# Performance work log

Measured on AMD Instinct MI355X. Metric: run time of the kernel, lower is better.

Reference implementation:

```python
import jax, jax.numpy as jnp
import numpy as np

NUM_HEADS = 8
NEG_LARGE = -1e9  # stands in for -inf under the causal mask; masked entries get exactly 0 entmax weight


def _entmax15(z):
    """Exact 1.5-entmax along the last axis (Peters & Martins 2019 sort-based algorithm)."""
    z = z * 0.5
    zs = -jnp.sort(-z, axis=-1)                      # descending sort
    T = z.shape[-1]
    k = jnp.arange(1, T + 1, dtype=z.dtype)
    mean = jnp.cumsum(zs, axis=-1) / k
    mean_sq = jnp.cumsum(zs * zs, axis=-1) / k
    ss = k * (mean_sq - mean * mean)
    delta = (1.0 - ss) / k
    tau = mean - jnp.sqrt(jnp.maximum(delta, 0.0))
    support = jnp.sum(tau <= zs, axis=-1, keepdims=True)      # support size >= 1
    tau_star = jnp.take_along_axis(tau, support - 1, axis=-1)
    return jnp.square(jnp.maximum(z - tau_star, 0.0))


def setup_inputs() -> dict:
    key = jax.random.key(0)
    ks = jax.random.split(key, 9)
    B, T, D, H = 2, 2048, 512, NUM_HEADS
    dk = D // H
    s = 1.0 / np.sqrt(D)
    so = 1.0 / np.sqrt(dk)
    x = jax.random.normal(ks[0], (B, T, D), jnp.float32)
    Wq = jax.random.uniform(ks[1], (D, D), jnp.float32, -s, s)
    bq = jax.random.uniform(ks[2], (D,), jnp.float32, -s, s)
    Wk = jax.random.uniform(ks[3], (D, D), jnp.float32, -s, s)
    bk = jax.random.uniform(ks[4], (D,), jnp.float32, -s, s)
    Wv = jax.random.uniform(ks[5], (D, D), jnp.float32, -s, s)
    bv = jax.random.uniform(ks[6], (D,), jnp.float32, -s, s)
    Wo = jax.random.uniform(ks[7], (dk, D), jnp.float32, -so, so)
    bo = jax.random.uniform(ks[8], (D,), jnp.float32, -so, so)
    return {"x": x, "Wq": Wq, "bq": bq, "Wk": Wk, "bk": bk, "Wv": Wv, "bv": bv, "Wo": Wo, "bo": bo}


def reference(x, Wq, bq, Wk, bk, Wv, bv, Wo, bo):
    B, T, D = x.shape
    H = NUM_HEADS
    dk = D // H
    Q = (x @ Wq + bq).reshape(B, T, H, dk).transpose(0, 2, 1, 3)   # [B,H,T,dk]
    K = (x @ Wk + bk).reshape(B, T, H, dk).transpose(0, 2, 1, 3)
    V = (x @ Wv + bv).reshape(B, T, H, dk).transpose(0, 2, 1, 3)
    scores = jnp.einsum('bhtd,bhsd->bhts', Q, K) / np.float32(np.sqrt(dk))
    causal = jnp.triu(jnp.ones((T, T), bool), k=1)                 # True above diagonal
    scores = jnp.where(causal[None, None, :, :], jnp.float32(NEG_LARGE), scores)
    weights = _entmax15(scores)                                    # [B,H,T,T]
    weights_avg = weights.mean(axis=1)                             # [B,T,T]
    V_combined = V.mean(axis=1)                                    # [B,T,dk]
    out = jnp.einsum('bts,bsd->btd', weights_avg, V_combined)      # [B,T,dk]
    return out @ Wo + bo, weights_avg
```

## Files before the change

kernel.cpp:

```cpp
#include <hip/hip_runtime.h>
#include <hip/hip_bf16.h>
#include <cstdint>

#define B_ 2
#define T_ 2048
#define D_ 512
#define H_ 8
#define DK_ 64
#define TQ_ 8
#define NTL_ (T_ / TQ_)
#define M_ (B_ * T_)

__global__ __launch_bounds__(256) void gemm_bias_kernel(
    const float* __restrict__ A, const float* __restrict__ W,
    const float* __restrict__ bias, float* __restrict__ C,
    int M, int N, int K)
{
  __shared__ float As[32][68];
  __shared__ float Bs[32][68];
  const int bm = blockIdx.y * 64;
  const int bn = blockIdx.x * 64;
  const int tid = threadIdx.x;
  const int tx = tid & 15, ty = tid >> 4;
  float acc[4][4] = {};
  for (int k0 = 0; k0 < K; k0 += 32) {
    {
      const int r = tid >> 2;
      const int c = (tid & 3) << 2;
      const float4 a0 = *reinterpret_cast<const float4*>(&A[(size_t)(bm + r) * K + k0 + c]);
      const float4 a1 = *reinterpret_cast<const float4*>(&A[(size_t)(bm + r) * K + k0 + 16 + c]);
      As[c + 0][r] = a0.x;  As[c + 1][r] = a0.y;  As[c + 2][r] = a0.z;  As[c + 3][r] = a0.w;
      As[c + 16][r] = a1.x; As[c + 17][r] = a1.y; As[c + 18][r] = a1.z; As[c + 19][r] = a1.w;
    }
    {
      const int r = tid >> 4;
      const int c = (tid & 15) << 2;
      *reinterpret_cast<float4*>(&Bs[r][c]) =
          *reinterpret_cast<const float4*>(&W[(size_t)(k0 + r) * N + bn + c]);
      *reinterpret_cast<float4*>(&Bs[r + 16][c]) =
          *reinterpret_cast<const float4*>(&W[(size_t)(k0 + 16 + r) * N + bn + c]);
    }
    __syncthreads();
#pragma unroll
    for (int kk = 0; kk < 32; ++kk) {
      const float4 av = *reinterpret_cast<const float4*>(&As[kk][ty * 4]);
      const float4 bv = *reinterpret_cast<const float4*>(&Bs[kk][tx * 4]);
      acc[0][0] = fmaf(av.x, bv.x, acc[0][0]); acc[0][1] = fmaf(av.x, bv.y, acc[0][1]);
      acc[0][2] = fmaf(av.x, bv.z, acc[0][2]); acc[0][3] = fmaf(av.x, bv.w, acc[0][3]);
      acc[1][0] = fmaf(av.y, bv.x, acc[1][0]); acc[1][1] = fmaf(av.y, bv.y, acc[1][1]);
      acc[1][2] = fmaf(av.y, bv.z, acc[1][2]); acc[1][3] = fmaf(av.y, bv.w, acc[1][3]);
      acc[2][0] = fmaf(av.z, bv.x, acc[2][0]); acc[2][1] = fmaf(av.z, bv.y, acc[2][1]);
      acc[2][2] = fmaf(av.z, bv.z, acc[2][2]); acc[2][3] = fmaf(av.z, bv.w, acc[2][3]);
      acc[3][0] = fmaf(av.w, bv.x, acc[3][0]); acc[3][1] = fmaf(av.w, bv.y, acc[3][1]);
      acc[3][2] = fmaf(av.w, bv.z, acc[3][2]); acc[3][3] = fmaf(av.w, bv.w, acc[3][3]);
    }
    __syncthreads();
  }
#pragma unroll
  for (int i = 0; i < 4; ++i) {
    const int row = bm + ty * 4 + i;
#pragma unroll
    for (int j = 0; j < 4; ++j) {
      const int col = bn + tx * 4 + j;
      C[(size_t)row * N + col] = acc[i][j] + bias[col];
    }
  }
}

__global__ __launch_bounds__(256) void gemm_bias_kernelT(
    const float* __restrict__ A, const float* __restrict__ W,
    const float* __restrict__ bias, float* __restrict__ Ct,
    int M, int N, int K)
{
  __shared__ float As[32][68];
  __shared__ float Bs[32][68];
  const int bm = blockIdx.y * 64;
  const int bn = blockIdx.x * 64;
  const int tid = threadIdx.x;
  const int tx = tid & 15, ty = tid >> 4;
  float acc[4][4] = {};
  for (int k0 = 0; k0 < K; k0 += 32) {
    {
      const int r = tid >> 2;
      const int c = (tid & 3) << 2;
      const float4 a0 = *reinterpret_cast<const float4*>(&A[(size_t)(bm + r) * K + k0 + c]);
      const float4 a1 = *reinterpret_cast<const float4*>(&A[(size_t)(bm + r) * K + k0 + 16 + c]);
      As[c + 0][r] = a0.x;  As[c + 1][r] = a0.y;  As[c + 2][r] = a0.z;  As[c + 3][r] = a0.w;
      As[c + 16][r] = a1.x; As[c + 17][r] = a1.y; As[c + 18][r] = a1.z; As[c + 19][r] = a1.w;
    }
    {
      const int r = tid >> 4;
      const int c = (tid & 15) << 2;
      *reinterpret_cast<float4*>(&Bs[r][c]) =
          *reinterpret_cast<const float4*>(&W[(size_t)(k0 + r) * N + bn + c]);
      *reinterpret_cast<float4*>(&Bs[r + 16][c]) =
          *reinterpret_cast<const float4*>(&W[(size_t)(k0 + 16 + r) * N + bn + c]);
    }
    __syncthreads();
#pragma unroll
    for (int kk = 0; kk < 32; ++kk) {
      const float4 av = *reinterpret_cast<const float4*>(&As[kk][ty * 4]);
      const float4 bv = *reinterpret_cast<const float4*>(&Bs[kk][tx * 4]);
      acc[0][0] = fmaf(av.x, bv.x, acc[0][0]); acc[0][1] = fmaf(av.x, bv.y, acc[0][1]);
      acc[0][2] = fmaf(av.x, bv.z, acc[0][2]); acc[0][3] = fmaf(av.x, bv.w, acc[0][3]);
      acc[1][0] = fmaf(av.y, bv.x, acc[1][0]); acc[1][1] = fmaf(av.y, bv.y, acc[1][1]);
      acc[1][2] = fmaf(av.y, bv.z, acc[1][2]); acc[1][3] = fmaf(av.y, bv.w, acc[1][3]);
      acc[2][0] = fmaf(av.z, bv.x, acc[2][0]); acc[2][1] = fmaf(av.z, bv.y, acc[2][1]);
      acc[2][2] = fmaf(av.z, bv.z, acc[2][2]); acc[2][3] = fmaf(av.z, bv.w, acc[2][3]);
      acc[3][0] = fmaf(av.w, bv.x, acc[3][0]); acc[3][1] = fmaf(av.w, bv.y, acc[3][1]);
      acc[3][2] = fmaf(av.w, bv.z, acc[3][2]); acc[3][3] = fmaf(av.w, bv.w, acc[3][3]);
    }
    __syncthreads();
  }
#pragma unroll
  for (int j = 0; j < 4; ++j) {
    const int col = bn + tx * 4 + j;
    const float bb = bias[col];
    const float4 v = make_float4(acc[0][j] + bb, acc[1][j] + bb, acc[2][j] + bb, acc[3][j] + bb);
    *reinterpret_cast<float4*>(&Ct[(size_t)col * M + bm + ty * 4]) = v;
  }
}

__global__ __launch_bounds__(256) void vcombine_kernel(const float* __restrict__ V,
                                                       float* __restrict__ Vc)
{
  const int idx = blockIdx.x * 256 + threadIdx.x;
  if (idx >= M_ * DK_) return;
  const int row = idx >> 6, d = idx & 63;
  float s = 0.f;
#pragma unroll
  for (int h = 0; h < H_; ++h) s += V[(size_t)row * D_ + h * DK_ + d];
  Vc[idx] = s * 0.125f;
}

__global__ __launch_bounds__(512, 4)
void attn_kernel(
    const float* __restrict__ Qg, const float* __restrict__ Kt,
    const float* __restrict__ Vc, float* __restrict__ wavg,
    float* __restrict__ attn_out)
{
  __shared__ float sc[TQ_][T_];
  __shared__ float part[4][TQ_][DK_];

  const int tid = threadIdx.x;
  const int b = blockIdx.x & 1;
  const int tile = (NTL_ - 1) - (blockIdx.x >> 1);
  const int t0 = tile * TQ_;
  const int nS = t0 + TQ_;
  const int wave = __builtin_amdgcn_readfirstlane(tid >> 6);
  const int lane = tid & 63;
  const int n = t0 + wave + 1;
  float* const scw = &sc[wave][0];

  float wacc[32];
#pragma unroll
  for (int j = 0; j < 32; ++j) wacc[j] = 0.f;

  for (int h = 0; h < H_; ++h) {
    if (wave * 256 < nS) {
      const int s0 = min(tid * 4, nS - 4);
      const float* Ktp = &Kt[(size_t)(h * DK_) * M_ + b * T_ + s0];
      const float* Qp  = &Qg[(size_t)(b * T_ + t0) * D_ + h * DK_];
      float4 a[TQ_];
#pragma unroll
      for (int r = 0; r < TQ_; ++r) a[r] = make_float4(0.f, 0.f, 0.f, 0.f);
#pragma unroll 2
      for (int d4 = 0; d4 < 16; ++d4) {
        const float4 k0 = *reinterpret_cast<const float4*>(Ktp + (size_t)(d4 * 4 + 0) * M_);
        const float4 k1 = *reinterpret_cast<const float4*>(Ktp + (size_t)(d4 * 4 + 1) * M_);
        const float4 k2 = *reinterpret_cast<const float4*>(Ktp + (size_t)(d4 * 4 + 2) * M_);
        const float4 k3 = *reinterpret_cast<const float4*>(Ktp + (size_t)(d4 * 4 + 3) * M_);
#pragma unroll
        for (int r = 0; r < TQ_; ++r) {
          const float q0 = Qp[r * D_ + d4 * 4 + 0];
          const float q1 = Qp[r * D_ + d4 * 4 + 1];
          const float q2 = Qp[r * D_ + d4 * 4 + 2];
          const float q3 = Qp[r * D_ + d4 * 4 + 3];
          a[r].x = fmaf(q0, k0.x, a[r].x); a[r].y = fmaf(q0, k0.y, a[r].y);
          a[r].z = fmaf(q0, k0.z, a[r].z); a[r].w = fmaf(q0, k0.w, a[r].w);
          a[r].x = fmaf(q1, k1.x, a[r].x); a[r].y = fmaf(q1, k1.y, a[r].y);
          a[r].z = fmaf(q1, k1.z, a[r].z); a[r].w = fmaf(q1, k1.w, a[r].w);
          a[r].x = fmaf(q2, k2.x, a[r].x); a[r].y = fmaf(q2, k2.y, a[r].y);
          a[r].z = fmaf(q2, k2.z, a[r].z); a[r].w = fmaf(q2, k2.w, a[r].w);
          a[r].x = fmaf(q3, k3.x, a[r].x); a[r].y = fmaf(q3, k3.y, a[r].y);
          a[r].z = fmaf(q3, k3.z, a[r].z); a[r].w = fmaf(q3, k3.w, a[r].w);
        }
      }
#pragma unroll
      for (int r = 0; r < TQ_; ++r) {
        a[r].x *= 0.0625f; a[r].y *= 0.0625f; a[r].z *= 0.0625f; a[r].w *= 0.0625f;
        *reinterpret_cast<float4*>(&sc[r][s0]) = a[r];
      }
    }
    __syncthreads();

    float srow[32];
#pragma unroll
    for (int j = 0; j < 32; ++j) {
      if (j * 64 < n) {
        const int s = lane + j * 64;
        const float v = scw[s];
        srow[j] = (s < n) ? v : -1e30f;
      }
    }

    float mx = -1e30f;
#pragma unroll
    for (int j = 0; j < 32; ++j)
      if (j * 64 < n) mx = fmaxf(mx, srow[j]);
#pragma unroll
    for (int m = 32; m >= 1; m >>= 1) mx = fmaxf(mx, __shfl_xor(mx, m, 64));

    float tau = mx - 1.0f;
#pragma unroll 1
    for (int it = 0; it < 12; ++it) {
      float s1 = 0.f, s2 = 0.f, cn = 0.f;
#pragma unroll
      for (int j = 0; j < 32; ++j) {
        if (j * 64 < n) {
          const float u = fmaxf(srow[j] - tau, 0.f);
          s1 += u;
          s2 = fmaf(u, u, s2);
          cn += (u > 0.f) ? 1.f : 0.f;
        }
      }
#pragma unroll
      for (int m = 32; m >= 1; m >>= 1) {
        s1 += __shfl_xor(s1, m, 64);
        s2 += __shfl_xor(s2, m, 64);
      }
      if (fabsf(s2 - 1.0f) < 1e-5f) break;
      if (it < 3) {
#pragma unroll
        for (int m = 32; m >= 1; m >>= 1) cn += __shfl_xor(cn, m, 64);
        const float kf = fmaxf(cn, 1.f);
        const float mu = tau + s1 / kf;
        const float ss = s2 - s1 * s1 / kf;
        tau = mu - sqrtf(fmaxf((1.0f - ss) / kf, 0.f));
      } else {
        tau += (s2 - 1.0f) / fmaxf(2.f * s1, 1e-12f);
      }
    }
    tau = fminf(tau, mx - 1e-8f);

#pragma unroll
    for (int j = 0; j < 32; ++j) {
      if (j * 64 < n) {
        const float u = fmaxf(srow[j] - tau, 0.f);
        wacc[j] = fmaf(u, u, wacc[j]);
      }
    }
    __syncthreads();
  }

#pragma unroll
  for (int j = 0; j < 32; ++j) scw[lane + j * 64] = wacc[j];
  __syncthreads();

  for (int i4 = tid; i4 < TQ_ * T_ / 4; i4 += 512) {
    const int r = i4 >> 9;
    const int c4 = i4 & 511;
    float4 w = reinterpret_cast<const float4*>(&sc[r][0])[c4];
    w.x *= 0.125f; w.y *= 0.125f; w.z *= 0.125f; w.w *= 0.125f;
    reinterpret_cast<float4*>(&wavg[(size_t)(b * T_ + t0 + r) * T_])[c4] = w;
  }

  {
    const int sg = wave & 3;
    const int rb = (wave >> 2) * 4;
    float a0 = 0.f, a1 = 0.f, a2 = 0.f, a3 = 0.f;
    for (int s = sg; s < nS; s += 4) {
      const float v = Vc[(size_t)(b * T_ + s) * DK_ + lane];
      a0 += sc[rb + 0][s] * v;
      a1 += sc[rb + 1][s] * v;
      a2 += sc[rb + 2][s] * v;
      a3 += sc[rb + 3][s] * v;
    }
    part[sg][rb + 0][lane] = a0;
    part[sg][rb + 1][lane] = a1;
    part[sg][rb + 2][lane] = a2;
    part[sg][rb + 3][lane] = a3;
  }
  __syncthreads();
  {
    const int r = wave;
    const float o = (part[0][r][lane] + part[1][r][lane] +
                     part[2][r][lane] + part[3][r][lane]) * 0.125f;
    attn_out[(size_t)(b * T_ + t0 + r) * DK_ + lane] = o;
  }
}

extern "C" void kernel_launch(void* const* d_in, const int* in_sizes, int n_in,
                              void* d_out, int out_size, void* d_ws, size_t ws_size,
                              hipStream_t stream)
{
  const float* x  = (const float*)d_in[0];
  const float* Wq = (const float*)d_in[1];
  const float* bq = (const float*)d_in[2];
  const float* Wk = (const float*)d_in[3];
  const float* bk = (const float*)d_in[4];
  const float* Wv = (const float*)d_in[5];
  const float* bv = (const float*)d_in[6];
  const float* Wo = (const float*)d_in[7];
  const float* bo = (const float*)d_in[8];
  float* out = (float*)d_out;
  float* ws  = (float*)d_ws;

  float* Q  = ws;
  float* Kt = Q + (size_t)M_ * D_;
  float* V  = Kt + (size_t)D_ * M_;
  float* Vc = V + (size_t)M_ * D_;
  float* AO = Vc + (size_t)M_ * DK_;

  float* out1 = out;
  float* wavg = out + (size_t)M_ * D_;

  const dim3 gp(D_ / 64, M_ / 64);
  gemm_bias_kernel <<<gp, 256, 0, stream>>>(x, Wq, bq, Q,  M_, D_, D_);
  gemm_bias_kernelT<<<gp, 256, 0, stream>>>(x, Wk, bk, Kt, M_, D_, D_);
  gemm_bias_kernel <<<gp, 256, 0, stream>>>(x, Wv, bv, V,  M_, D_, D_);
  vcombine_kernel<<<(M_ * DK_ + 255) / 256, 256, 0, stream>>>(V, Vc);
  attn_kernel<<<B_ * NTL_, 512, 0, stream>>>(Q, Kt, Vc, wavg, AO);
  gemm_bias_kernel<<<gp, 256, 0, stream>>>(AO, Wo, bo, out1, M_, D_, DK_);
}
```

Before: 376.4 us.

## Warp-specialize attention: producer waves compute next head scores while consumers run entmax

Halves the query tile to four rows and double-buffers the score tile in shared memory. Waves 0-3 compute QK scores for head h+1 while waves 4-7 each run the entmax threshold iteration on one row for head h, so score computation overlaps with the serial entmax solve. This removes the phase where all waves sat idle waiting on either step. In exchange, twice as many blocks reload K per head with a smaller tile (less Q reuse), and half the waves idle in each role when the workloads are unbalanced.

```diff
diff --git a/kernel.cpp b/kernel.cpp
--- a/kernel.cpp
+++ b/kernel.cpp
@@ -7,7 +7,7 @@
 #define D_ 512
 #define H_ 8
 #define DK_ 64
-#define TQ_ 8
+#define TQ_ 4
 #define NTL_ (T_ / TQ_)
 #define M_ (B_ * T_)
 
@@ -139,7 +139,7 @@
     const float* __restrict__ Vc, float* __restrict__ wavg,
     float* __restrict__ attn_out)
 {
-  __shared__ float sc[TQ_][T_];
+  __shared__ float sc[2][TQ_][T_];
   __shared__ float part[4][TQ_][DK_];
 
   const int tid = threadIdx.x;
@@ -149,140 +149,153 @@
   const int nS = t0 + TQ_;
   const int wave = __builtin_amdgcn_readfirstlane(tid >> 6);
   const int lane = tid & 63;
-  const int n = t0 + wave + 1;
-  float* const scw = &sc[wave][0];
 
   float wacc[32];
 #pragma unroll
   for (int j = 0; j < 32; ++j) wacc[j] = 0.f;
 
+  auto score_head = [&](int h, int nb) {
+    const int stid = (wave << 6) | lane;
+    const float* Qp = &Qg[(size_t)(b * T_ + t0) * D_ + h * DK_];
+#pragma unroll 1
+    for (int c = 0; c < T_; c += 1024) {
+      if (c < nS) {
+        const int s0 = min(stid * 4 + c, nS - 4);
+        const float* Ktp = &Kt[(size_t)(h * DK_) * M_ + b * T_ + s0];
+        float4 a0 = {}, a1 = {}, a2 = {}, a3 = {};
+#pragma unroll 2
+        for (int d4 = 0; d4 < 16; ++d4) {
+          const float4 k0 = *reinterpret_cast<const float4*>(Ktp + (size_t)(d4 * 4 + 0) * M_);
+          const float4 k1 = *reinterpret_cast<const float4*>(Ktp + (size_t)(d4 * 4 + 1) * M_);
+          const float4 k2 = *reinterpret_cast<const float4*>(Ktp + (size_t)(d4 * 4 + 2) * M_);
+          const float4 k3 = *reinterpret_cast<const float4*>(Ktp + (size_t)(d4 * 4 + 3) * M_);
+#pragma unroll
+          for (int r = 0; r < TQ_; ++r) {
+            const float q0 = Qp[r * D_ + d4 * 4 + 0];
+            const float q1 = Qp[r * D_ + d4 * 4 + 1];
+            const float q2 = Qp[r * D_ + d4 * 4 + 2];
+            const float q3 = Qp[r * D_ + d4 * 4 + 3];
+            float4& a = (r == 0) ? a0 : (r == 1) ? a1 : (r == 2) ? a2 : a3;
+            a.x = fmaf(q0, k0.x, a.x); a.y = fmaf(q0, k0.y, a.y);
+            a.z = fmaf(q0, k0.z, a.z); a.w = fmaf(q0, k0.w, a.w);
+            a.x = fmaf(q1, k1.x, a.x); a.y = fmaf(q1, k1.y, a.y);
+            a.z = fmaf(q1, k1.z, a.z); a.w = fmaf(q1, k1.w, a.w);
+            a.x = fmaf(q2, k2.x, a.x); a.y = fmaf(q2, k2.y, a.y);
+            a.z = fmaf(q2, k2.z, a.z); a.w = fmaf(q2, k2.w, a.w);
+            a.x = fmaf(q3, k3.x, a.x); a.y = fmaf(q3, k3.y, a.y);
+            a.z = fmaf(q3, k3.z, a.z); a.w = fmaf(q3, k3.w, a.w);
+          }
+        }
+        a0.x *= 0.0625f; a0.y *= 0.0625f; a0.z *= 0.0625f; a0.w *= 0.0625f;
+        a1.x *= 0.0625f; a1.y *= 0.0625f; a1.z *= 0.0625f; a1.w *= 0.0625f;
+        a2.x *= 0.0625f; a2.y *= 0.0625f; a2.z *= 0.0625f; a2.w *= 0.0625f;
+        a3.x *= 0.0625f; a3.y *= 0.0625f; a3.z *= 0.0625f; a3.w *= 0.0625f;
+        *reinterpret_cast<float4*>(&sc[nb][0][s0]) = a0;
+        *reinterpret_cast<float4*>(&sc[nb][1][s0]) = a1;
+        *reinterpret_cast<float4*>(&sc[nb][2][s0]) = a2;
+        *reinterpret_cast<float4*>(&sc[nb][3][s0]) = a3;
+      }
+    }
+  };
+
+  if (wave < 4) score_head(0, 0);
+  __syncthreads();
+
+#pragma unroll 1
   for (int h = 0; h < H_; ++h) {
-    if (wave * 256 < nS) {
-      const int s0 = min(tid * 4, nS - 4);
-      const float* Ktp = &Kt[(size_t)(h * DK_) * M_ + b * T_ + s0];
-      const float* Qp  = &Qg[(size_t)(b * T_ + t0) * D_ + h * DK_];
-      float4 a[TQ_];
-#pragma unroll
-      for (int r = 0; r < TQ_; ++r) a[r] = make_float4(0.f, 0.f, 0.f, 0.f);
-#pragma unroll 2
-      for (int d4 = 0; d4 < 16; ++d4) {
-        const float4 k0 = *reinterpret_cast<const float4*>(Ktp + (size_t)(d4 * 4 + 0) * M_);
-        const float4 k1 = *reinterpret_cast<const float4*>(Ktp + (size_t)(d4 * 4 + 1) * M_);
-        const float4 k2 = *reinterpret_cast<const float4*>(Ktp + (size_t)(d4 * 4 + 2) * M_);
-        const float4 k3 = *reinterpret_cast<const float4*>(Ktp + (size_t)(d4 * 4 + 3) * M_);
-#pragma unroll
-        for (int r = 0; r < TQ_; ++r) {
-          const float q0 = Qp[r * D_ + d4 * 4 + 0];
-          const float q1 = Qp[r * D_ + d4 * 4 + 1];
-          const float q2 = Qp[r * D_ + d4 * 4 + 2];
-          const float q3 = Qp[r * D_ + d4 * 4 + 3];
-          a[r].x = fmaf(q0, k0.x, a[r].x); a[r].y = fmaf(q0, k0.y, a[r].y);
-          a[r].z = fmaf(q0, k0.z, a[r].z); a[r].w = fmaf(q0, k0.w, a[r].w);
-          a[r].x = fmaf(q1, k1.x, a[r].x); a[r].y = fmaf(q1, k1.y, a[r].y);
-          a[r].z = fmaf(q1, k1.z, a[r].z); a[r].w = fmaf(q1, k1.w, a[r].w);
-          a[r].x = fmaf(q2, k2.x, a[r].x); a[r].y = fmaf(q2, k2.y, a[r].y);
-          a[r].z = fmaf(q2, k2.z, a[r].z); a[r].w = fmaf(q2, k2.w, a[r].w);
-          a[r].x = fmaf(q3, k3.x, a[r].x); a[r].y = fmaf(q3, k3.y, a[r].y);
-          a[r].z = fmaf(q3, k3.z, a[r].z); a[r].w = fmaf(q3, k3.w, a[r].w);
+    if (wave < 4) {
+      if (h + 1 < H_) score_head(h + 1, (h + 1) & 1);
+    } else {
+      const int row = wave - 4;
+      const int n = t0 + row + 1;
+      const float* scw = &sc[h & 1][row][0];
+
+      float srow[32];
+      float mx = -1e30f;
+#pragma unroll
+      for (int j = 0; j < 32; ++j) {
+        if (j * 64 < n) {
+          const int s = lane + j * 64;
+          const float v = (s < n) ? scw[s] : -1e30f;
+          srow[j] = v;
+          mx = fmaxf(mx, v);
         }
       }
 #pragma unroll
-      for (int r = 0; r < TQ_; ++r) {
-        a[r].x *= 0.0625f; a[r].y *= 0.0625f; a[r].z *= 0.0625f; a[r].w *= 0.0625f;
-        *reinterpret_cast<float4*>(&sc[r][s0]) = a[r];
+      for (int m = 32; m >= 1; m >>= 1) mx = fmaxf(mx, __shfl_xor(mx, m, 64));
+
+      float tau = mx - 1.0f;
+#pragma unroll 1
+      for (int it = 0; it < 12; ++it) {
+        float s1 = 0.f, s2 = 0.f, cn = 0.f;
+#pragma unroll
+        for (int j = 0; j < 32; ++j) {
+          if (j * 64 < n) {
+            const float u = fmaxf(srow[j] - tau, 0.f);
+            s1 += u;
+            s2 = fmaf(u, u, s2);
+            cn += (u > 0.f) ? 1.f : 0.f;
+          }
+        }
+#pragma unroll
+        for (int m = 32; m >= 1; m >>= 1) {
+          s1 += __shfl_xor(s1, m, 64);
+          s2 += __shfl_xor(s2, m, 64);
+        }
+        if (fabsf(s2 - 1.0f) < 1e-5f) break;
+        if (it < 3) {
+#pragma unroll
+          for (int m = 32; m >= 1; m >>= 1) cn += __shfl_xor(cn, m, 64);
+          const float kf = fmaxf(cn, 1.f);
+          const float mu = tau + s1 / kf;
+          const float ss = s2 - s1 * s1 / kf;
+          tau = mu - sqrtf(fmaxf((1.0f - ss) / kf, 0.f));
+        } else {
+          tau += (s2 - 1.0f) / fmaxf(2.f * s1, 1e-12f);
+        }
       }
-    }
-    __syncthreads();
-
-    float srow[32];
-#pragma unroll
-    for (int j = 0; j < 32; ++j) {
-      if (j * 64 < n) {
-        const int s = lane + j * 64;
-        const float v = scw[s];
-        srow[j] = (s < n) ? v : -1e30f;
-      }
-    }
-
-    float mx = -1e30f;
-#pragma unroll
-    for (int j = 0; j < 32; ++j)
-      if (j * 64 < n) mx = fmaxf(mx, srow[j]);
-#pragma unroll
-    for (int m = 32; m >= 1; m >>= 1) mx = fmaxf(mx, __shfl_xor(mx, m, 64));
-
-    float tau = mx - 1.0f;
-#pragma unroll 1
-    for (int it = 0; it < 12; ++it) {
-      float s1 = 0.f, s2 = 0.f, cn = 0.f;
+      tau = fminf(tau, mx - 1e-8f);
+
 #pragma unroll
       for (int j = 0; j < 32; ++j) {
         if (j * 64 < n) {
           const float u = fmaxf(srow[j] - tau, 0.f);
-          s1 += u;
-          s2 = fmaf(u, u, s2);
-          cn += (u > 0.f) ? 1.f : 0.f;
+          wacc[j] = fmaf(u, u, wacc[j]);
         }
       }
-#pragma unroll
-      for (int m = 32; m >= 1; m >>= 1) {
-        s1 += __shfl_xor(s1, m, 64);
-        s2 += __shfl_xor(s2, m, 64);
-      }
-      if (fabsf(s2 - 1.0f) < 1e-5f) break;
-      if (it < 3) {
-#pragma unroll
-        for (int m = 32; m >= 1; m >>= 1) cn += __shfl_xor(cn, m, 64);
-        const float kf = fmaxf(cn, 1.f);
-        const float mu = tau + s1 / kf;
-        const float ss = s2 - s1 * s1 / kf;
-        tau = mu - sqrtf(fmaxf((1.0f - ss) / kf, 0.f));
-      } else {
-        tau += (s2 - 1.0f) / fmaxf(2.f * s1, 1e-12f);
-      }
-    }
-    tau = fminf(tau, mx - 1e-8f);
-
-#pragma unroll
-    for (int j = 0; j < 32; ++j) {
-      if (j * 64 < n) {
-        const float u = fmaxf(srow[j] - tau, 0.f);
-        wacc[j] = fmaf(u, u, wacc[j]);
-      }
-    }
-    __syncthreads();
-  }
-
-#pragma unroll
-  for (int j = 0; j < 32; ++j) scw[lane + j * 64] = wacc[j];
+    }
+    __syncthreads();
+  }
+
+  if (wave >= 4) {
+    const int row = wave - 4;
+#pragma unroll
+    for (int j = 0; j < 32; ++j) sc[0][row][lane + j * 64] = wacc[j];
+  }
   __syncthreads();
 
   for (int i4 = tid; i4 < TQ_ * T_ / 4; i4 += 512) {
     const int r = i4 >> 9;
     const int c4 = i4 & 511;
-    float4 w = reinterpret_cast<const float4*>(&sc[r][0])[c4];
+    float4 w = reinterpret_cast<const float4*>(&sc[0][r][0])[c4];
     w.x *= 0.125f; w.y *= 0.125f; w.z *= 0.125f; w.w *= 0.125f;
     reinterpret_cast<float4*>(&wavg[(size_t)(b * T_ + t0 + r) * T_])[c4] = w;
   }
 
   {
     const int sg = wave & 3;
-    const int rb = (wave >> 2) * 4;
-    float a0 = 0.f, a1 = 0.f, a2 = 0.f, a3 = 0.f;
+    const int rp = (wave >> 2) * 2;
+    float a0 = 0.f, a1 = 0.f;
     for (int s = sg; s < nS; s += 4) {
       const float v = Vc[(size_t)(b * T_ + s) * DK_ + lane];
-      a0 += sc[rb + 0][s] * v;
-      a1 += sc[rb + 1][s] * v;
-      a2 += sc[rb + 2][s] * v;
-      a3 += sc[rb + 3][s] * v;
-    }
-    part[sg][rb + 0][lane] = a0;
-    part[sg][rb + 1][lane] = a1;
-    part[sg][rb + 2][lane] = a2;
-    part[sg][rb + 3][lane] = a3;
+      a0 += sc[0][rp + 0][s] * v;
+      a1 += sc[0][rp + 1][s] * v;
+    }
+    part[sg][rp + 0][lane] = a0;
+    part[sg][rp + 1][lane] = a1;
   }
   __syncthreads();
-  {
+  if (wave < TQ_) {
     const int r = wave;
     const float o = (part[0][r][lane] + part[1][r][lane] +
                      part[2][r][lane] + part[3][r][lane]) * 0.125f;
```

Measured after the change: 533.9 us. 1.42x slower.

## Split attention per head with int16 scores, atomic weight accumulation, separate PV kernel

Applied to the files above, without the earlier changes.

The attention kernel is restructured so each block handles one head, one batch and a 4-row query tile. This multiplies the grid by the head count and shrinks shared memory by storing scores as quantized int16 in a scaled domain. Per-head entmax weights are accumulated into a pre-zeroed wavg buffer with sparse atomicAdds (only nonzero entries). The weights-times-V product moves to a new pv_kernel that reads wavg back from global memory. This adds a zeroing pass, atomic traffic and an extra global read of the 32MB weight matrix. The int16 quantization of scores (step 1/512) also risks accuracy loss.

```diff
diff --git a/kernel.cpp b/kernel.cpp
--- a/kernel.cpp
+++ b/kernel.cpp
@@ -7,9 +7,12 @@
 #define D_ 512
 #define H_ 8
 #define DK_ 64
-#define TQ_ 8
+#define TQ_ 4
 #define NTL_ (T_ / TQ_)
 #define M_ (B_ * T_)
+
+#define SSC_ 8192.0f
+#define S2_  (SSC_ * SSC_)
 
 __global__ __launch_bounds__(256) void gemm_bias_kernel(
     const float* __restrict__ A, const float* __restrict__ W,
@@ -133,160 +136,196 @@
   Vc[idx] = s * 0.125f;
 }
 
-__global__ __launch_bounds__(512, 4)
+__global__ __launch_bounds__(256) void zero_kernel(float4* __restrict__ p, int n4)
+{
+  const int stride = gridDim.x * 256;
+  const float4 z = make_float4(0.f, 0.f, 0.f, 0.f);
+  for (int i = blockIdx.x * 256 + threadIdx.x; i < n4; i += stride) p[i] = z;
+}
+
+__global__ __launch_bounds__(256, 6)
 void attn_kernel(
     const float* __restrict__ Qg, const float* __restrict__ Kt,
-    const float* __restrict__ Vc, float* __restrict__ wavg,
-    float* __restrict__ attn_out)
-{
-  __shared__ float sc[TQ_][T_];
-  __shared__ float part[4][TQ_][DK_];
+    float* __restrict__ wavg)
+{
+  __shared__ short ssc[TQ_][T_];
 
   const int tid = threadIdx.x;
-  const int b = blockIdx.x & 1;
-  const int tile = (NTL_ - 1) - (blockIdx.x >> 1);
+  const int bid = blockIdx.x;
+  const int h = bid >> 10;
+  const int b = (bid >> 9) & 1;
+  const int tile = (NTL_ - 1) - (bid & 511);
   const int t0 = tile * TQ_;
   const int nS = t0 + TQ_;
   const int wave = __builtin_amdgcn_readfirstlane(tid >> 6);
   const int lane = tid & 63;
-  const int n = t0 + wave + 1;
-  float* const scw = &sc[wave][0];
-
-  float wacc[32];
-#pragma unroll
-  for (int j = 0; j < 32; ++j) wacc[j] = 0.f;
-
-  for (int h = 0; h < H_; ++h) {
-    if (wave * 256 < nS) {
-      const int s0 = min(tid * 4, nS - 4);
-      const float* Ktp = &Kt[(size_t)(h * DK_) * M_ + b * T_ + s0];
-      const float* Qp  = &Qg[(size_t)(b * T_ + t0) * D_ + h * DK_];
-      float4 a[TQ_];
-#pragma unroll
-      for (int r = 0; r < TQ_; ++r) a[r] = make_float4(0.f, 0.f, 0.f, 0.f);
+
+  {
+    const float* Qp = &Qg[(size_t)(b * T_ + t0) * D_ + h * DK_];
+#pragma unroll 1
+    for (int c = 0; c < T_; c += 1024) {
+      if (c < nS) {
+        const int s0 = min(tid * 4 + c, nS - 4);
+        const float* Ktp = &Kt[(size_t)(h * DK_) * M_ + b * T_ + s0];
+        float4 a[TQ_];
+#pragma unroll
+        for (int r = 0; r < TQ_; ++r) a[r] = make_float4(0.f, 0.f, 0.f, 0.f);
 #pragma unroll 2
-      for (int d4 = 0; d4 < 16; ++d4) {
-        const float4 k0 = *reinterpret_cast<const float4*>(Ktp + (size_t)(d4 * 4 + 0) * M_);
-        const float4 k1 = *reinterpret_cast<const float4*>(Ktp + (size_t)(d4 * 4 + 1) * M_);
-        const float4 k2 = *reinterpret_cast<const float4*>(Ktp + (size_t)(d4 * 4 + 2) * M_);
-        const float4 k3 = *reinterpret_cast<const float4*>(Ktp + (size_t)(d4 * 4 + 3) * M_);
+        for (int d4 = 0; d4 < 16; ++d4) {
+          const float4 k0 = *reinterpret_cast<const float4*>(Ktp + (size_t)(d4 * 4 + 0) * M_);
+          const float4 k1 = *reinterpret_cast<const float4*>(Ktp + (size_t)(d4 * 4 + 1) * M_);
+          const float4 k2 = *reinterpret_cast<const float4*>(Ktp + (size_t)(d4 * 4 + 2) * M_);
+          const float4 k3 = *reinterpret_cast<const float4*>(Ktp + (size_t)(d4 * 4 + 3) * M_);
+#pragma unroll
+          for (int r = 0; r < TQ_; ++r) {
+            const float q0 = Qp[r * D_ + d4 * 4 + 0];
+            const float q1 = Qp[r * D_ + d4 * 4 + 1];
+            const float q2 = Qp[r * D_ + d4 * 4 + 2];
+            const float q3 = Qp[r * D_ + d4 * 4 + 3];
+            a[r].x = fmaf(q0, k0.x, a[r].x); a[r].y = fmaf(q0, k0.y, a[r].y);
+            a[r].z = fmaf(q0, k0.z, a[r].z); a[r].w = fmaf(q0, k0.w, a[r].w);
+            a[r].x = fmaf(q1, k1.x, a[r].x); a[r].y = fmaf(q1, k1.y, a[r].y);
+            a[r].z = fmaf(q1, k1.z, a[r].z); a[r].w = fmaf(q1, k1.w, a[r].w);
+            a[r].x = fmaf(q2, k2.x, a[r].x); a[r].y = fmaf(q2, k2.y, a[r].y);
+            a[r].z = fmaf(q2, k2.z, a[r].z); a[r].w = fmaf(q2, k2.w, a[r].w);
+            a[r].x = fmaf(q3, k3.x, a[r].x); a[r].y = fmaf(q3, k3.y, a[r].y);
+            a[r].z = fmaf(q3, k3.z, a[r].z); a[r].w = fmaf(q3, k3.w, a[r].w);
+          }
+        }
 #pragma unroll
         for (int r = 0; r < TQ_; ++r) {
-          const float q0 = Qp[r * D_ + d4 * 4 + 0];
-          const float q1 = Qp[r * D_ + d4 * 4 + 1];
-          const float q2 = Qp[r * D_ + d4 * 4 + 2];
-          const float q3 = Qp[r * D_ + d4 * 4 + 3];
-          a[r].x = fmaf(q0, k0.x, a[r].x); a[r].y = fmaf(q0, k0.y, a[r].y);
-          a[r].z = fmaf(q0, k0.z, a[r].z); a[r].w = fmaf(q0, k0.w, a[r].w);
-          a[r].x = fmaf(q1, k1.x, a[r].x); a[r].y = fmaf(q1, k1.y, a[r].y);
-          a[r].z = fmaf(q1, k1.z, a[r].z); a[r].w = fmaf(q1, k1.w, a[r].w);
-          a[r].x = fmaf(q2, k2.x, a[r].x); a[r].y = fmaf(q2, k2.y, a[r].y);
-          a[r].z = fmaf(q2, k2.z, a[r].z); a[r].w = fmaf(q2, k2.w, a[r].w);
-          a[r].x = fmaf(q3, k3.x, a[r].x); a[r].y = fmaf(q3, k3.y, a[r].y);
-          a[r].z = fmaf(q3, k3.z, a[r].z); a[r].w = fmaf(q3, k3.w, a[r].w);
+          const int i0 = __float2int_rn(fminf(fmaxf(a[r].x * 512.f, -32000.f), 32000.f));
+          const int i1 = __float2int_rn(fminf(fmaxf(a[r].y * 512.f, -32000.f), 32000.f));
+          const int i2 = __float2int_rn(fminf(fmaxf(a[r].z * 512.f, -32000.f), 32000.f));
+          const int i3 = __float2int_rn(fminf(fmaxf(a[r].w * 512.f, -32000.f), 32000.f));
+          short4 st; st.x = (short)i0; st.y = (short)i1; st.z = (short)i2; st.w = (short)i3;
+          *reinterpret_cast<short4*>(&ssc[r][s0]) = st;
         }
       }
-#pragma unroll
-      for (int r = 0; r < TQ_; ++r) {
-        a[r].x *= 0.0625f; a[r].y *= 0.0625f; a[r].z *= 0.0625f; a[r].w *= 0.0625f;
-        *reinterpret_cast<float4*>(&sc[r][s0]) = a[r];
+    }
+  }
+  __syncthreads();
+
+  const int t = t0 + wave;
+  const int n = t + 1;
+  float srow[32];
+
+#pragma unroll
+  for (int j = 0; j < 4; ++j) {
+    if (j * 512 < n) {
+      const uint4 pk = *reinterpret_cast<const uint4*>(&ssc[wave][j * 512 + lane * 8]);
+      const unsigned pw[4] = {pk.x, pk.y, pk.z, pk.w};
+#pragma unroll
+      for (int q = 0; q < 4; ++q) {
+        const int s_lo = j * 512 + lane * 8 + q * 2;
+        const float lo = (float)((int)(short)(pw[q] & 0xffffu));
+        const float hi = (float)((int)pw[q] >> 16);
+        srow[j * 8 + q * 2 + 0] = (s_lo + 0 < n) ? lo : -1e30f;
+        srow[j * 8 + q * 2 + 1] = (s_lo + 1 < n) ? hi : -1e30f;
       }
-    }
-    __syncthreads();
-
-    float srow[32];
-#pragma unroll
-    for (int j = 0; j < 32; ++j) {
-      if (j * 64 < n) {
-        const int s = lane + j * 64;
-        const float v = scw[s];
-        srow[j] = (s < n) ? v : -1e30f;
-      }
-    }
-
-    float mx = -1e30f;
-#pragma unroll
-    for (int j = 0; j < 32; ++j)
-      if (j * 64 < n) mx = fmaxf(mx, srow[j]);
-#pragma unroll
-    for (int m = 32; m >= 1; m >>= 1) mx = fmaxf(mx, __shfl_xor(mx, m, 64));
-
-    float tau = mx - 1.0f;
+    } else {
+#pragma unroll
+      for (int q = 0; q < 8; ++q) srow[j * 8 + q] = -1e30f;
+    }
+  }
+  asm volatile("" ::: "memory");
+
+  float mx = -1e30f;
+#pragma unroll
+  for (int i = 0; i < 32; ++i) mx = fmaxf(mx, srow[i]);
+#pragma unroll
+  for (int m = 32; m >= 1; m >>= 1) mx = fmaxf(mx, __shfl_xor(mx, m, 64));
+
+  float tau = mx - SSC_;
 #pragma unroll 1
-    for (int it = 0; it < 12; ++it) {
-      float s1 = 0.f, s2 = 0.f, cn = 0.f;
-#pragma unroll
-      for (int j = 0; j < 32; ++j) {
-        if (j * 64 < n) {
-          const float u = fmaxf(srow[j] - tau, 0.f);
+  for (int it = 0; it < 12; ++it) {
+    float s1 = 0.f, s2 = 0.f, cn = 0.f;
+#pragma unroll
+    for (int j = 0; j < 4; ++j) {
+      if (j * 512 < n) {
+#pragma unroll
+        for (int q = 0; q < 8; ++q) {
+          const float u = fmaxf(srow[j * 8 + q] - tau, 0.f);
           s1 += u;
           s2 = fmaf(u, u, s2);
           cn += (u > 0.f) ? 1.f : 0.f;
         }
       }
-#pragma unroll
-      for (int m = 32; m >= 1; m >>= 1) {
-        s1 += __shfl_xor(s1, m, 64);
-        s2 += __shfl_xor(s2, m, 64);
+    }
+#pragma unroll
+    for (int m = 32; m >= 1; m >>= 1) {
+      s1 += __shfl_xor(s1, m, 64);
+      s2 += __shfl_xor(s2, m, 64);
+    }
+    if (fabsf(s2 - S2_) < 672.f) break;
+    if (it < 3) {
+#pragma unroll
+      for (int m = 32; m >= 1; m >>= 1) cn += __shfl_xor(cn, m, 64);
+      const float kf = fmaxf(cn, 1.f);
+      const float mu = tau + s1 / kf;
+      const float ss = s2 - s1 * s1 / kf;
+      tau = mu - sqrtf(fmaxf((S2_ - ss) / kf, 0.f));
+    } else {
+      tau += (s2 - S2_) / fmaxf(2.f * s1, 1e-6f);
+    }
+  }
+  tau = fminf(tau, mx - 1.f);
+
+  const float wconv = 0.125f / (SSC_ * SSC_);
+  float* const wrow = &wavg[(size_t)(b * T_ + t) * T_];
+#pragma unroll
+  for (int j = 0; j < 4; ++j) {
+    if (j * 512 < n) {
+#pragma unroll
+      for (int q = 0; q < 8; ++q) {
+        const float u = fmaxf(srow[j * 8 + q] - tau, 0.f);
+        if (__any(u > 0.f)) {
+          if (u > 0.f) {
+            const int s = j * 512 + lane * 8 + q;
+            atomicAdd(&wrow[s], u * u * wconv);
+          }
+        }
       }
-      if (fabsf(s2 - 1.0f) < 1e-5f) break;
-      if (it < 3) {
-#pragma unroll
-        for (int m = 32; m >= 1; m >>= 1) cn += __shfl_xor(cn, m, 64);
-        const float kf = fmaxf(cn, 1.f);
-        const float mu = tau + s1 / kf;
-        const float ss = s2 - s1 * s1 / kf;
-        tau = mu - sqrtf(fmaxf((1.0f - ss) / kf, 0.f));
-      } else {
-        tau += (s2 - 1.0f) / fmaxf(2.f * s1, 1e-12f);
-      }
-    }
-    tau = fminf(tau, mx - 1e-8f);
-
-#pragma unroll
-    for (int j = 0; j < 32; ++j) {
-      if (j * 64 < n) {
-        const float u = fmaxf(srow[j] - tau, 0.f);
-        wacc[j] = fmaf(u, u, wacc[j]);
-      }
-    }
-    __syncthreads();
-  }
-
-#pragma unroll
-  for (int j = 0; j < 32; ++j) scw[lane + j * 64] = wacc[j];
-  __syncthreads();
-
-  for (int i4 = tid; i4 < TQ_ * T_ / 4; i4 += 512) {
-    const int r = i4 >> 9;
-    const int c4 = i4 & 511;
-    float4 w = reinterpret_cast<const float4*>(&sc[r][0])[c4];
-    w.x *= 0.125f; w.y *= 0.125f; w.z *= 0.125f; w.w *= 0.125f;
-    reinterpret_cast<float4*>(&wavg[(size_t)(b * T_ + t0 + r) * T_])[c4] = w;
-  }
-
-  {
-    const int sg = wave & 3;
-    const int rb = (wave >> 2) * 4;
-    float a0 = 0.f, a1 = 0.f, a2 = 0.f, a3 = 0.f;
-    for (int s = sg; s < nS; s += 4) {
-      const float v = Vc[(size_t)(b * T_ + s) * DK_ + lane];
-      a0 += sc[rb + 0][s] * v;
-      a1 += sc[rb + 1][s] * v;
-      a2 += sc[rb + 2][s] * v;
-      a3 += sc[rb + 3][s] * v;
-    }
-    part[sg][rb + 0][lane] = a0;
-    part[sg][rb + 1][lane] = a1;
-    part[sg][rb + 2][lane] = a2;
-    part[sg][rb + 3][lane] = a3;
-  }
+    }
+  }
+}
+
+__global__ __launch_bounds__(256) void pv_kernel(
+    const float* __restrict__ wavg, const float* __restrict__ Vc,
+    float* __restrict__ AO)
+{
+  __shared__ float part[4][TQ_][DK_];
+  const int tid = threadIdx.x;
+  const int m0 = blockIdx.x * TQ_;
+  const int b = m0 >> 11;
+  const int tl = m0 & (T_ - 1);
+  const int wave = __builtin_amdgcn_readfirstlane(tid >> 6);
+  const int lane = tid & 63;
+
+  const int smax = min((wave + 1) * 512, tl + TQ_);
+  float a0 = 0.f, a1 = 0.f, a2 = 0.f, a3 = 0.f;
+  const float* w0 = &wavg[(size_t)(m0 + 0) * T_];
+  const float* w1 = &wavg[(size_t)(m0 + 1) * T_];
+  const float* w2 = &wavg[(size_t)(m0 + 2) * T_];
+  const float* w3 = &wavg[(size_t)(m0 + 3) * T_];
+#pragma unroll 1
+  for (int s = wave * 512; s < smax; ++s) {
+    const float v = Vc[(size_t)(b * T_ + s) * DK_ + lane];
+    a0 = fmaf(w0[s], v, a0);
+    a1 = fmaf(w1[s], v, a1);
+    a2 = fmaf(w2[s], v, a2);
+    a3 = fmaf(w3[s], v, a3);
+  }
+  part[wave][0][lane] = a0;
+  part[wave][1][lane] = a1;
+  part[wave][2][lane] = a2;
+  part[wave][3][lane] = a3;
   __syncthreads();
   {
     const int r = wave;
-    const float o = (part[0][r][lane] + part[1][r][lane] +
-                     part[2][r][lane] + part[3][r][lane]) * 0.125f;
-    attn_out[(size_t)(b * T_ + t0 + r) * DK_ + lane] = o;
+    const float o = part[0][r][lane] + part[1][r][lane] +
+                    part[2][r][lane] + part[3][r][lane];
+    AO[(size_t)(m0 + r) * DK_ + lane] = o;
   }
 }
 
@@ -320,6 +359,11 @@
   gemm_bias_kernelT<<<gp, 256, 0, stream>>>(x, Wk, bk, Kt, M_, D_, D_);
   gemm_bias_kernel <<<gp, 256, 0, stream>>>(x, Wv, bv, V,  M_, D_, D_);
   vcombine_kernel<<<(M_ * DK_ + 255) / 256, 256, 0, stream>>>(V, Vc);
-  attn_kernel<<<B_ * NTL_, 512, 0, stream>>>(Q, Kt, Vc, wavg, AO);
+
+  zero_kernel<<<2048, 256, 0, stream>>>(reinterpret_cast<float4*>(wavg),
+                                        (int)((size_t)B_ * T_ * T_ / 4));
+
+  attn_kernel<<<H_ * B_ * NTL_, 256, 0, stream>>>(Q, Kt, wavg);
+  pv_kernel<<<M_ / TQ_, 256, 0, stream>>>(wavg, Vc, AO);
   gemm_bias_kernel<<<gp, 256, 0, stream>>>(AO, Wo, bo, out1, M_, D_, DK_);
 }
```

After: 439.5 us. +16.8%, slower.
